# Optimization experiments

Measured on AMD Instinct MI355X. Metric: run time of the kernel, lower is better.

Reference implementation:

```python
import jax, jax.numpy as jnp
import numpy as np

NEG_INF = -1e30  # finite stand-in for -inf (fp16/bf16-safe)


def _ctc_loss(log_probs, labels):
    """CTC negative log-likelihood per example (blank index = 0).

    log_probs: [T, B, V] log-softmaxed logits (time-major, as tf.nn.ctc_loss default)
    labels:    [B, L] int labels in [1, V)
    returns:   [B] per-example loss
    """
    T, B, V = log_probs.shape
    L = labels.shape[1]
    S = 2 * L + 1  # blank-interleaved extended label length
    ext = jnp.zeros((B, S), labels.dtype).at[:, 1::2].set(labels)  # b_l1_b_l2_..._b
    # skip transition (s-2 -> s) allowed iff ext[s] != blank and ext[s] != ext[s-2]
    skip = jnp.concatenate(
        [jnp.zeros((B, 2), bool),
         (ext[:, 2:] != 0) & (ext[:, 2:] != ext[:, :-2])], axis=1)  # [B, S]

    def emit(lp_t):  # gather emission log-probs at extended label ids: [B,V]->[B,S]
        return jnp.take_along_axis(lp_t, ext, axis=1)

    # alpha[0]: only first blank and first label are reachable
    alpha0 = jnp.where(jnp.arange(S) < 2, emit(log_probs[0]), NEG_INF)  # [B, S]

    def step(alpha, lp_t):
        a1 = jnp.pad(alpha[:, :-1], ((0, 0), (1, 0)), constant_values=NEG_INF)
        a2 = jnp.pad(alpha[:, :-2], ((0, 0), (2, 0)), constant_values=NEG_INF)
        a2 = jnp.where(skip, a2, NEG_INF)
        m = jnp.maximum(jnp.maximum(alpha, a1), a2)  # stable 3-way logsumexp
        comb = m + jnp.log(jnp.exp(alpha - m) + jnp.exp(a1 - m) + jnp.exp(a2 - m))
        return comb + emit(lp_t), None

    alphaT, _ = jax.lax.scan(step, alpha0, log_probs[1:])
    # valid terminal states: last blank or last label
    return -jnp.logaddexp(alphaT[:, -1], alphaT[:, -2])  # [B]


def setup_inputs() -> dict:
    key = jax.random.key(0)
    k1, k2 = jax.random.split(key)
    T, B, V, L = 512, 1024, 96, 48
    y_pred = jax.random.normal(k1, (T, B, V), dtype=jnp.float32)  # time-major logits
    y_true = jax.random.randint(k2, (B, L), 1, V, dtype=jnp.int32)  # avoid blank=0
    return {"y_true": y_true, "y_pred": y_pred}


def reference(y_true, y_pred):
    log_probs = jax.nn.log_softmax(y_pred, axis=-1)
    return jnp.mean(_ctc_loss(log_probs, y_true))
```

## Files before the change

kernel.cpp:

```cpp
#include <hip/hip_runtime.h>

#define TT 512
#define BB 1024
#define VV 96
#define LL 48

__device__ __forceinline__ int f2i(float x) { return __float_as_int(x); }
__device__ __forceinline__ float i2f(int x) { return __int_as_float(x); }

template <int CTRL, int RM, int BM, bool BC>
__device__ __forceinline__ float dppf(float old, float src) {
    return i2f(__builtin_amdgcn_update_dpp(f2i(old), f2i(src), CTRL, RM, BM, BC));
}

__device__ __forceinline__ float wave_sum(float v) {
    v += dppf<0xB1, 0xF, 0xF, true>(0.f, v);
    v += dppf<0x4E, 0xF, 0xF, true>(0.f, v);
    v += dppf<0x141, 0xF, 0xF, true>(0.f, v);
    v += dppf<0x140, 0xF, 0xF, true>(0.f, v);
    v += dppf<0x142, 0xA, 0xF, false>(0.f, v);
    v += dppf<0x143, 0xC, 0xF, false>(0.f, v);
    return i2f(__builtin_amdgcn_readlane(f2i(v), 63));
}

__device__ __forceinline__ float wave_max(float v) {
    v = fmaxf(v, dppf<0xB1, 0xF, 0xF, true>(0.f, v));
    v = fmaxf(v, dppf<0x4E, 0xF, 0xF, true>(0.f, v));
    v = fmaxf(v, dppf<0x141, 0xF, 0xF, true>(0.f, v));
    v = fmaxf(v, dppf<0x140, 0xF, 0xF, true>(0.f, v));
    v = fmaxf(v, dppf<0x142, 0xA, 0xF, false>(0.f, v));
    v = fmaxf(v, dppf<0x143, 0xC, 0xF, false>(0.f, v));
    return i2f(__builtin_amdgcn_readlane(f2i(v), 63));
}

__global__ __launch_bounds__(128) void ctc_fused_split(
        const int* __restrict__ labels,
        const float* __restrict__ yp,
        float* __restrict__ loss) {
    const int b = blockIdx.x;
    const int tid = threadIdx.x;
    const int wid = tid >> 6;
    const int l = tid & 63;
    const int* lb = labels + b * LL;

    const bool odd = (l & 1);
    const int i0 = l >> 1;
    int i1 = (63 + l) >> 1; if (i1 > LL - 1) i1 = LL - 1;
    const int la0 = lb[i0];
    const int lp0 = lb[(i0 > 0) ? i0 - 1 : 0];
    const int la1 = lb[i1];
    const int lp1 = lb[(i1 > 0) ? i1 - 1 : 0];
    const bool v1 = (l <= 32);
    const bool skip0 = odd && (l >= 3) && (la0 != lp0);
    const bool skip1 = odd && v1 && (la1 != lp1);
    int i0n = i0 + 1; if (i0n > LL - 1) i0n = LL - 1;
    int i1n = i1 + 1; if (i1n > LL - 1) i1n = LL - 1;
    const bool skT0 = odd && (lb[i0n] != la0);
    const bool skT1 = odd && (l < 31) && (lb[i1n] != la1);

    const int id0 = odd ? la0 : 0;
    const int id1 = (odd && v1) ? la1 : 0;
    const int pa0 = (id0 >> 1) << 2, ps0 = id0 & 1;
    const int pa1 = (id1 >> 1) << 2, ps1 = id1 & 1;

    const int cl = (l < 48) ? l : 47;
    const float2* rowp = (const float2*)yp + (size_t)b * (VV / 2) + cl;
    const size_t step2 = (size_t)BB * (VV / 2);

    float2 ring[8];
    float A0, A1;
    int S2 = 0;
    float EP0, EP1;

#define STAGEA(r, EO0, EO1) { \
        float ex0 = __expf((r).x), ex1 = __expf((r).y); \
        float se = (l < 48) ? (ex0 + ex1) : 0.f; \
        float tot = wave_sum(se); \
        float r96 = 96.0f * __builtin_amdgcn_rcpf(tot); \
        float g0x = i2f(__builtin_amdgcn_ds_bpermute(pa0, f2i(ex0))); \
        float g0y = i2f(__builtin_amdgcn_ds_bpermute(pa0, f2i(ex1))); \
        float g1x = i2f(__builtin_amdgcn_ds_bpermute(pa1, f2i(ex0))); \
        float g1y = i2f(__builtin_amdgcn_ds_bpermute(pa1, f2i(ex1))); \
        EO0 = (ps0 ? g0y : g0x) * r96; \
        EO1 = (ps1 ? g1y : g1x) * r96; }

#define RENORM { \
        float vm = fmaxf(A0, v1 ? A1 : 0.f); \
        float m = wave_max(vm); \
        int ebits = (f2i(m) >> 23) & 0xFF; \
        float sc = i2f((254 - ebits) << 23); \
        A0 *= sc; \
        A1 = v1 ? A1 * sc : 0.f; \
        S2 += ebits - 127; }

    __shared__ float sB0[64];
    __shared__ float sB1[33];
    __shared__ int sS2b;

    if (wid == 0) {
        #pragma unroll
        for (int j = 0; j < 8; ++j) ring[j] = rowp[(size_t)j * step2];
        A0 = (l == 0) ? 1.f : 0.f;
        A1 = 0.f;
        STAGEA(ring[0], EP0, EP1);
        ring[0] = rowp[(size_t)8 * step2];
        for (int o = 0; o < 8; ++o) {
            for (int u = 0; u < 4; ++u) {
                #pragma unroll
                for (int tt = 0; tt < 8; ++tt) {
                    const int k = 32 * o + 8 * u + tt;
                    float a1_0 = dppf<0x138, 0xF, 0xF, false>(0.f, A0);
                    float a2_0 = dppf<0x138, 0xF, 0xF, false>(0.f, a1_0);
                    float b63 = i2f(__builtin_amdgcn_readlane(f2i(A0), 63));
                    float b62 = i2f(__builtin_amdgcn_readlane(f2i(A0), 62));
                    float a1_1 = dppf<0x138, 0xF, 0xF, false>(b63, A1);
                    float a2_1 = dppf<0x138, 0xF, 0xF, false>(b62, a1_1);
                    A0 = (A0 + a1_0 + (skip0 ? a2_0 : 0.f)) * EP0;
                    A1 = (A1 + a1_1 + (skip1 ? a2_1 : 0.f)) * EP1;
                    STAGEA(ring[(tt + 1) & 7], EP0, EP1);
                    int kr = k + 9; if (kr > 255) kr = 255;
                    ring[(tt + 1) & 7] = rowp[(size_t)kr * step2];
                }
            }
            RENORM
        }
    } else {
        #pragma unroll
        for (int j = 0; j < 8; ++j) ring[j] = rowp[(size_t)(511 - j) * step2];
        A0 = 0.f;
        A1 = (l == 31 || l == 32) ? 1.f : 0.f;
        STAGEA(ring[0], EP0, EP1);
        ring[0] = rowp[(size_t)(511 - 8) * step2];
        for (int o = 0; o < 8; ++o) {
            for (int u = 0; u < 4; ++u) {
                #pragma unroll
                for (int tt = 0; tt < 8; ++tt) {
                    const int k = 32 * o + 8 * u + tt;
                    float w0 = A0 * EP0;
                    float w1 = A1 * EP1;
                    float t0 = i2f(__builtin_amdgcn_readlane(f2i(w1), 0));
                    float t1 = i2f(__builtin_amdgcn_readlane(f2i(w1), 1));
                    float s1_0 = dppf<0x130, 0xF, 0xF, false>(t0, w0);
                    float s2_0 = dppf<0x130, 0xF, 0xF, false>(t1, s1_0);
                    float s1_1 = dppf<0x130, 0xF, 0xF, false>(0.f, w1);
                    float s2_1 = dppf<0x130, 0xF, 0xF, false>(0.f, s1_1);
                    A0 = w0 + s1_0 + (skT0 ? s2_0 : 0.f);
                    A1 = w1 + s1_1 + (skT1 ? s2_1 : 0.f);
                    STAGEA(ring[(tt + 1) & 7], EP0, EP1);
                    int kr = k + 9; if (kr > 255) kr = 255;
                    ring[(tt + 1) & 7] = rowp[(size_t)(511 - kr) * step2];
                }
            }
            RENORM
        }
        sB0[l] = A0;
        if (l < 33) sB1[l] = A1;
        if (l == 0) sS2b = S2;
    }
    __syncthreads();
    if (wid == 0) {
        const int lc = (l < 33) ? l : 32;
        double pd = (double)A0 * (double)sB0[l];
        pd += v1 ? (double)A1 * (double)sB1[lc] : 0.0;
        #pragma unroll
        for (int m = 1; m < 64; m <<= 1) pd += __shfl_xor(pd, m);
        if (l == 0) {
            long long ud = __double_as_longlong(pd);
            int eb = (int)((ud >> 52) & 0x7FF);
            double md = __longlong_as_double(
                (ud & 0x000FFFFFFFFFFFFFLL) | 0x3FF0000000000000LL);
            int s2tot = S2 + sS2b + (eb - 1023);
            loss[b] = 2336.946274031532f
                    - (float)s2tot * 0.6931471805599453f
                    - __logf((float)md);
        }
    }
#undef STAGEA
#undef RENORM
}

__global__ __launch_bounds__(256) void ctc_mean_kernel(
        const float* __restrict__ loss, float* __restrict__ out) {
    const int tid = threadIdx.x;
    float v = loss[tid] + loss[tid + 256] + loss[tid + 512] + loss[tid + 768];
    #pragma unroll
    for (int m = 1; m < 64; m <<= 1) v += __shfl_xor(v, m);
    __shared__ float part[4];
    if ((tid & 63) == 0) part[tid >> 6] = v;
    __syncthreads();
    if (tid == 0) out[0] = (part[0] + part[1] + part[2] + part[3]) * (1.0f / (float)BB);
}

extern "C" void kernel_launch(void* const* d_in, const int* in_sizes, int n_in,
                              void* d_out, int out_size, void* d_ws, size_t ws_size,
                              hipStream_t stream) {
    const int* y_true = (const int*)d_in[0];
    const float* y_pred = (const float*)d_in[1];
    float* out = (float*)d_out;
    float* lossbuf = (float*)d_ws;

    ctc_fused_split<<<BB, 128, 0, stream>>>(y_true, y_pred, lossbuf);
    ctc_mean_kernel<<<1, 256, 0, stream>>>(lossbuf, out);
}
```

Baseline: 283.2 us.

## Pack blank/label CTC states per lane and gather label emissions directly

Each lane now holds one blank state and one label state (lane l: blank before label l, and label l), in place of two strided halves of the extended sequence. This removes the cross-half readlanes and the second DPP shift chain. Label emissions are fetched with a direct scalar gather from global memory rather than four ds_bpermute shuffles per step. The blank emission is broadcast with readfirstlane. This cuts per-step cross-lane work on the serial recurrence, but adds an extra per-lane uncoalesced global load for each timestep.

Result: no change. 285.2 us (+0.7%).

```diff
diff --git a/kernel.cpp b/kernel.cpp
--- a/kernel.cpp
+++ b/kernel.cpp
@@ -33,7 +33,7 @@
     return i2f(__builtin_amdgcn_readlane(f2i(v), 63));
 }
 
-__global__ __launch_bounds__(128) void ctc_fused_split(
+__global__ __launch_bounds__(128) void ctc_split_packed(
         const int* __restrict__ labels,
         const float* __restrict__ yp,
         float* __restrict__ loss) {
@@ -43,125 +43,102 @@
     const int l = tid & 63;
     const int* lb = labels + b * LL;
 
-    const bool odd = (l & 1);
-    const int i0 = l >> 1;
-    int i1 = (63 + l) >> 1; if (i1 > LL - 1) i1 = LL - 1;
-    const int la0 = lb[i0];
-    const int lp0 = lb[(i0 > 0) ? i0 - 1 : 0];
-    const int la1 = lb[i1];
-    const int lp1 = lb[(i1 > 0) ? i1 - 1 : 0];
-    const bool v1 = (l <= 32);
-    const bool skip0 = odd && (l >= 3) && (la0 != lp0);
-    const bool skip1 = odd && v1 && (la1 != lp1);
-    int i0n = i0 + 1; if (i0n > LL - 1) i0n = LL - 1;
-    int i1n = i1 + 1; if (i1n > LL - 1) i1n = LL - 1;
-    const bool skT0 = odd && (lb[i0n] != la0);
-    const bool skT1 = odd && (l < 31) && (lb[i1n] != la1);
+    const int ll = (l < 48) ? l : 47;
+    const int lbl = lb[ll];
+    const bool lab = (l < 48);
+    const bool skF = (l >= 1) && lab && (lb[l - 1] != lbl);
+    const bool skB = (l < 47) && (lb[l + 1] != lbl);
 
-    const int id0 = odd ? la0 : 0;
-    const int id1 = (odd && v1) ? la1 : 0;
-    const int pa0 = (id0 >> 1) << 2, ps0 = id0 & 1;
-    const int pa1 = (id1 >> 1) << 2, ps1 = id1 & 1;
+    const float* base = yp + (size_t)b * VV;
+    const size_t rstep = (size_t)BB * VV;
 
-    const int cl = (l < 48) ? l : 47;
-    const float2* rowp = (const float2*)yp + (size_t)b * (VV / 2) + cl;
-    const size_t step2 = (size_t)BB * (VV / 2);
+    float2 ringD[8];
+    float  ringL[8];
+    float Ae, Ao;
+    int S2 = 0;
+    float Eb, El;
 
-    float2 ring[8];
-    float A0, A1;
-    int S2 = 0;
-    float EP0, EP1;
+#define LOADROW(ROW, SLOT) { \
+        const float* rp_ = base + (size_t)(ROW) * rstep; \
+        ringD[SLOT] = *(const float2*)(rp_ + 2 * ll); \
+        ringL[SLOT] = rp_[lbl]; }
 
-#define STAGEA(r, EO0, EO1) { \
-        float ex0 = __expf((r).x), ex1 = __expf((r).y); \
-        float se = (l < 48) ? (ex0 + ex1) : 0.f; \
+#define STAGEA(SLOT) { \
+        float ex0 = __expf(ringD[SLOT].x), ex1 = __expf(ringD[SLOT].y); \
+        float exl = __expf(ringL[SLOT]); \
+        float se = lab ? (ex0 + ex1) : 0.f; \
         float tot = wave_sum(se); \
         float r96 = 96.0f * __builtin_amdgcn_rcpf(tot); \
-        float g0x = i2f(__builtin_amdgcn_ds_bpermute(pa0, f2i(ex0))); \
-        float g0y = i2f(__builtin_amdgcn_ds_bpermute(pa0, f2i(ex1))); \
-        float g1x = i2f(__builtin_amdgcn_ds_bpermute(pa1, f2i(ex0))); \
-        float g1y = i2f(__builtin_amdgcn_ds_bpermute(pa1, f2i(ex1))); \
-        EO0 = (ps0 ? g0y : g0x) * r96; \
-        EO1 = (ps1 ? g1y : g1x) * r96; }
+        Eb = i2f(__builtin_amdgcn_readfirstlane(f2i(ex0))) * r96; \
+        El = lab ? exl * r96 : 0.f; }
 
 #define RENORM { \
-        float vm = fmaxf(A0, v1 ? A1 : 0.f); \
+        float vm = fmaxf(Ae, Ao); \
         float m = wave_max(vm); \
-        int ebits = (f2i(m) >> 23) & 0xFF; \
-        float sc = i2f((254 - ebits) << 23); \
-        A0 *= sc; \
-        A1 = v1 ? A1 * sc : 0.f; \
-        S2 += ebits - 127; }
+        int eb_ = (f2i(m) >> 23) & 0xFF; \
+        float sc = i2f((254 - eb_) << 23); \
+        Ae *= sc; Ao *= sc; \
+        S2 += eb_ - 127; }
 
-    __shared__ float sB0[64];
-    __shared__ float sB1[33];
+    __shared__ float sBe[64];
+    __shared__ float sBo[64];
     __shared__ int sS2b;
 
     if (wid == 0) {
         #pragma unroll
-        for (int j = 0; j < 8; ++j) ring[j] = rowp[(size_t)j * step2];
-        A0 = (l == 0) ? 1.f : 0.f;
-        A1 = 0.f;
-        STAGEA(ring[0], EP0, EP1);
-        ring[0] = rowp[(size_t)8 * step2];
+        for (int j = 0; j < 8; ++j) LOADROW(j, j)
+        Ae = (l == 0) ? 1.f : 0.f;
+        Ao = 0.f;
+        STAGEA(0)
+        LOADROW(8, 0)
         for (int o = 0; o < 8; ++o) {
             for (int u = 0; u < 4; ++u) {
                 #pragma unroll
                 for (int tt = 0; tt < 8; ++tt) {
                     const int k = 32 * o + 8 * u + tt;
-                    float a1_0 = dppf<0x138, 0xF, 0xF, false>(0.f, A0);
-                    float a2_0 = dppf<0x138, 0xF, 0xF, false>(0.f, a1_0);
-                    float b63 = i2f(__builtin_amdgcn_readlane(f2i(A0), 63));
-                    float b62 = i2f(__builtin_amdgcn_readlane(f2i(A0), 62));
-                    float a1_1 = dppf<0x138, 0xF, 0xF, false>(b63, A1);
-                    float a2_1 = dppf<0x138, 0xF, 0xF, false>(b62, a1_1);
-                    A0 = (A0 + a1_0 + (skip0 ? a2_0 : 0.f)) * EP0;
-                    A1 = (A1 + a1_1 + (skip1 ? a2_1 : 0.f)) * EP1;
-                    STAGEA(ring[(tt + 1) & 7], EP0, EP1);
+                    float sh = dppf<0x138, 0xF, 0xF, false>(0.f, Ao);
+                    float AeN = (Ae + sh) * Eb;
+                    float AoN = (Ao + Ae + (skF ? sh : 0.f)) * El;
+                    Ae = AeN; Ao = AoN;
+                    STAGEA((tt + 1) & 7)
                     int kr = k + 9; if (kr > 255) kr = 255;
-                    ring[(tt + 1) & 7] = rowp[(size_t)kr * step2];
+                    LOADROW(kr, (tt + 1) & 7)
                 }
             }
             RENORM
         }
     } else {
         #pragma unroll
-        for (int j = 0; j < 8; ++j) ring[j] = rowp[(size_t)(511 - j) * step2];
-        A0 = 0.f;
-        A1 = (l == 31 || l == 32) ? 1.f : 0.f;
-        STAGEA(ring[0], EP0, EP1);
-        ring[0] = rowp[(size_t)(511 - 8) * step2];
+        for (int j = 0; j < 8; ++j) LOADROW(511 - j, j)
+        Ae = (l == 48) ? 1.f : 0.f;
+        Ao = (l == 47) ? 1.f : 0.f;
+        STAGEA(0)
+        LOADROW(511 - 8, 0)
         for (int o = 0; o < 8; ++o) {
             for (int u = 0; u < 4; ++u) {
                 #pragma unroll
                 for (int tt = 0; tt < 8; ++tt) {
                     const int k = 32 * o + 8 * u + tt;
-                    float w0 = A0 * EP0;
-                    float w1 = A1 * EP1;
-                    float t0 = i2f(__builtin_amdgcn_readlane(f2i(w1), 0));
-                    float t1 = i2f(__builtin_amdgcn_readlane(f2i(w1), 1));
-                    float s1_0 = dppf<0x130, 0xF, 0xF, false>(t0, w0);
-                    float s2_0 = dppf<0x130, 0xF, 0xF, false>(t1, s1_0);
-                    float s1_1 = dppf<0x130, 0xF, 0xF, false>(0.f, w1);
-                    float s2_1 = dppf<0x130, 0xF, 0xF, false>(0.f, s1_1);
-                    A0 = w0 + s1_0 + (skT0 ? s2_0 : 0.f);
-                    A1 = w1 + s1_1 + (skT1 ? s2_1 : 0.f);
-                    STAGEA(ring[(tt + 1) & 7], EP0, EP1);
+                    float wE = Ae * Eb;
+                    float wO = Ao * El;
+                    float sE = dppf<0x130, 0xF, 0xF, false>(0.f, wE);
+                    float sO = dppf<0x130, 0xF, 0xF, false>(0.f, wO);
+                    Ae = wE + wO;
+                    Ao = wO + sE + (skB ? sO : 0.f);
+                    STAGEA((tt + 1) & 7)
                     int kr = k + 9; if (kr > 255) kr = 255;
-                    ring[(tt + 1) & 7] = rowp[(size_t)(511 - kr) * step2];
+                    LOADROW(511 - kr, (tt + 1) & 7)
                 }
             }
             RENORM
         }
-        sB0[l] = A0;
-        if (l < 33) sB1[l] = A1;
+        sBe[l] = Ae;
+        sBo[l] = Ao;
         if (l == 0) sS2b = S2;
     }
     __syncthreads();
     if (wid == 0) {
-        const int lc = (l < 33) ? l : 32;
-        double pd = (double)A0 * (double)sB0[l];
-        pd += v1 ? (double)A1 * (double)sB1[lc] : 0.0;
+        double pd = (double)Ae * (double)sBe[l] + (double)Ao * (double)sBo[l];
         #pragma unroll
         for (int m = 1; m < 64; m <<= 1) pd += __shfl_xor(pd, m);
         if (l == 0) {
@@ -175,6 +152,7 @@
                     - __logf((float)md);
         }
     }
+#undef LOADROW
 #undef STAGEA
 #undef RENORM
 }
@@ -199,6 +177,6 @@
     float* out = (float*)d_out;
     float* lossbuf = (float*)d_ws;
 
-    ctc_fused_split<<<BB, 128, 0, stream>>>(y_true, y_pred, lossbuf);
+    ctc_split_packed<<<BB, 128, 0, stream>>>(y_true, y_pred, lossbuf);
     ctc_mean_kernel<<<1, 256, 0, stream>>>(lossbuf, out);
 }
```
